# Kernel tuning notes

Measured on AMD Instinct MI355X. Metric: run time of the kernel, lower is better.

The kernel has to match this reference:

```python
import jax, jax.numpy as jnp
import numpy as np

TOP_K = 2


def setup_inputs() -> dict:
    key = jax.random.key(0)
    k0, k1, k2, k3 = jax.random.split(key, 4)
    B, S, H, I, E = 4, 2048, 1024, 2048, 8
    x = jax.random.normal(k0, (B, S, H), dtype=jnp.float32)
    Wr = jax.random.normal(k1, (H, E), dtype=jnp.float32) * 0.02
    W1 = jax.random.normal(k2, (E, H, 2 * I), dtype=jnp.float32) * 0.02
    W2 = jax.random.normal(k3, (E, I, H), dtype=jnp.float32) * 0.02
    return {"x": x, "Wr": Wr, "W1": W1, "W2": W2}


def reference(x, Wr, W1, W2):
    B, S, H = x.shape
    E = W1.shape[0]
    I = W2.shape[1]
    xf = x.reshape(-1, H)  # [T, H], T = B*S

    # Top-k router
    logits = xf @ Wr                              # [T, E]
    probs = jax.nn.softmax(logits, axis=-1)
    rw, sel = jax.lax.top_k(probs, TOP_K)          # [T, k], [T, k]
    rw = rw.astype(jnp.float32)
    rw = rw / rw.sum(axis=-1, keepdims=True)

    out = jnp.zeros_like(xf)
    for e in range(E):
        # combined gate weight for this expert per token (0 if not routed here)
        g = (rw * (sel == e)).sum(axis=-1)         # [T]
        h = xf @ W1[e]                             # [T, 2I]
        gate, up = h[:, :I], h[:, I:]
        eo = (jax.nn.silu(gate) * up) @ W2[e]      # [T, H]
        out = out + g[:, None] * eo
    return out.reshape(B, S, H)
```

## Files before the change

### kernel.cpp

```cpp
#include <hip/hip_runtime.h>
#include <hip/hip_bf16.h>

#define NTOK   8192
#define HDIM   1024
#define NEXP   8
#define IDIM   2048
#define TOTAL  (NTOK*2)

typedef short bf16x8 __attribute__((ext_vector_type(8)));
typedef float f32x4  __attribute__((ext_vector_type(4)));

__device__ __forceinline__ unsigned short f2bf(float f) {
  __hip_bfloat16 h = __float2bfloat16(f);
  return *reinterpret_cast<unsigned short*>(&h);
}
__device__ __forceinline__ float bf2f(unsigned short u) {
  __hip_bfloat16 h = *reinterpret_cast<__hip_bfloat16*>(&u);
  return __bfloat162float(h);
}

__device__ __forceinline__ void lds_load16(const unsigned short* gsrc, unsigned short* lds_base_uniform) {
  __builtin_amdgcn_global_load_lds(
      (const __attribute__((address_space(1))) unsigned int*)gsrc,
      (__attribute__((address_space(3))) unsigned int*)lds_base_uniform,
      16, 0, 0);
}

__global__ void router_kernel(const float* __restrict__ x, const float* __restrict__ Wr,
                              int* __restrict__ sel, float* __restrict__ selw,
                              int* __restrict__ counts) {
  int t = blockIdx.x * 4 + (threadIdx.x >> 6);
  int lane = threadIdx.x & 63;
  float acc[NEXP];
#pragma unroll
  for (int e = 0; e < NEXP; ++e) acc[e] = 0.f;
  const float* xr = x + (size_t)t * HDIM;
  for (int h = lane; h < HDIM; h += 64) {
    float xv = xr[h];
    const float* wr = Wr + h * NEXP;
#pragma unroll
    for (int e = 0; e < NEXP; ++e) acc[e] += xv * wr[e];
  }
#pragma unroll
  for (int off = 32; off > 0; off >>= 1) {
#pragma unroll
    for (int e = 0; e < NEXP; ++e) acc[e] += __shfl_xor(acc[e], off, 64);
  }
  if (lane == 0) {
    int i0 = 0; float v0 = acc[0];
#pragma unroll
    for (int e = 1; e < NEXP; ++e) if (acc[e] > v0) { v0 = acc[e]; i0 = e; }
    int i1 = -1; float v1 = -1e30f;
#pragma unroll
    for (int e = 0; e < NEXP; ++e) if (e != i0 && acc[e] > v1) { v1 = acc[e]; i1 = e; }
    float e1 = expf(v1 - v0);
    float w0 = 1.f / (1.f + e1);
    float w1 = e1 / (1.f + e1);
    sel[t*2] = i0; sel[t*2+1] = i1;
    selw[t*2] = w0; selw[t*2+1] = w1;
    atomicAdd(&counts[i0], 1);
    atomicAdd(&counts[i1], 1);
  }
}

__global__ void prefix_kernel(const int* __restrict__ counts, int* __restrict__ offsets,
                              int* __restrict__ cursor) {
  if (threadIdx.x == 0) {
    int s = 0;
    for (int e = 0; e < NEXP; ++e) { offsets[e] = s; cursor[e] = s; s += counts[e]; }
    offsets[NEXP] = s;
  }
}

__global__ void scatter_kernel(const int* __restrict__ sel, const float* __restrict__ selw,
                               int* __restrict__ cursor, int* __restrict__ token_ids,
                               float* __restrict__ gates) {
  int t = blockIdx.x * 256 + threadIdx.x;
  if (t >= NTOK) return;
#pragma unroll
  for (int k = 0; k < 2; ++k) {
    int e = sel[t*2+k];
    int p = atomicAdd(&cursor[e], 1);
    token_ids[p] = t;
    gates[p] = selw[t*2+k];
  }
}

__global__ void xsplit_kernel(const float* __restrict__ x, unsigned short* __restrict__ Xs) {
  int t = blockIdx.x;
  const float4* src = reinterpret_cast<const float4*>(x + (size_t)t * HDIM);
  float4 v = src[threadIdx.x];
  unsigned short h0 = f2bf(v.x), h1 = f2bf(v.y), h2 = f2bf(v.z), h3 = f2bf(v.w);
  ushort4 hi = { h0, h1, h2, h3 };
  ushort4 lo = { f2bf(v.x - bf2f(h0)), f2bf(v.y - bf2f(h1)),
                 f2bf(v.z - bf2f(h2)), f2bf(v.w - bf2f(h3)) };
  *reinterpret_cast<ushort4*>(Xs + (size_t)t*2*HDIM + threadIdx.x*4) = hi;
  *reinterpret_cast<ushort4*>(Xs + (size_t)t*2*HDIM + HDIM + threadIdx.x*4) = lo;
}

__global__ void split_transpose_kernel(const float* __restrict__ W, unsigned short* __restrict__ WT,
                                       int R, int C) {
  int e = blockIdx.z;
  int c0 = blockIdx.x * 64, r0 = blockIdx.y * 64;
  __shared__ unsigned short hiT[64][65];
  __shared__ unsigned short loT[64][65];
  int tx = threadIdx.x & 63, ty = threadIdx.x >> 6;
  const float* src = W + ((size_t)e * R + r0) * C + c0;
#pragma unroll
  for (int rr = 0; rr < 16; ++rr) {
    int r_l = ty * 16 + rr;
    float v = src[(size_t)r_l * C + tx];
    unsigned short h = f2bf(v);
    hiT[tx][r_l] = h;
    loT[tx][r_l] = f2bf(v - bf2f(h));
  }
  __syncthreads();
  unsigned short* dst = WT + ((size_t)e * C + c0) * (size_t)(2*R) + r0;
#pragma unroll
  for (int ww = 0; ww < 16; ++ww) {
    int c_l = ty * 16 + ww;
    dst[(size_t)c_l * (2*R) + tx]     = hiT[c_l][tx];
    dst[(size_t)c_l * (2*R) + R + tx] = loT[c_l][tx];
  }
}

__global__ __launch_bounds__(256, 2)
void gemm1_kernel(const unsigned short* __restrict__ Xs,
                  const unsigned short* __restrict__ W1sT,
                  unsigned short* __restrict__ actS,
                  const int* __restrict__ offsets,
                  const int* __restrict__ token_ids) {
  int e = blockIdx.z;
  int off = offsets[e];
  int cnt = offsets[e+1] - off;
  int r0 = blockIdx.x * 128;
  if (r0 >= cnt) return;
  int j0 = blockIdx.y * 128;

  __shared__ unsigned short As[128*64];
  __shared__ unsigned short Bg[128*64];
  __shared__ unsigned short Bu[128*64];

  int tid = threadIdx.x;
  int lane = tid & 63, wv = tid >> 6;
  int l15 = lane & 15, lq = lane >> 4;
  int lr = lane >> 3;
  int g  = lane & 7;
  int wr = wv >> 1;
  int wc = wv & 1;

  const unsigned short* w1e = W1sT + (size_t)e * 4096 * 2048;

  const unsigned short* srcA[4]; unsigned short* dstA[4];
  const unsigned short* srcBg[4]; const unsigned short* srcBu[4];
  unsigned short* dstBg[4]; unsigned short* dstBu[4];
#pragma unroll
  for (int i = 0; i < 4; ++i) {
    int rowt = wv*32 + i*8 + lr;
    int gp = off + r0 + rowt; if (gp > TOTAL-1) gp = TOTAL-1;
    int tok = token_ids[gp];
    int sg = g ^ (rowt & 7);
    srcA[i] = Xs + (size_t)tok*2048 + sg*8;
    dstA[i] = As + wv*2048 + i*512;
    srcBg[i] = w1e + (size_t)(j0 + rowt)*2048 + sg*8;
    srcBu[i] = w1e + (size_t)(IDIM + j0 + rowt)*2048 + sg*8;
    dstBg[i] = Bg + wv*2048 + i*512;
    dstBu[i] = Bu + wv*2048 + i*512;
  }

  f32x4 accg[4][4], accu[4][4];
#pragma unroll
  for (int m = 0; m < 4; ++m)
#pragma unroll
    for (int n = 0; n < 4; ++n) {
      accg[m][n] = f32x4{0.f, 0.f, 0.f, 0.f};
      accu[m][n] = f32x4{0.f, 0.f, 0.f, 0.f};
    }

  for (int ks = 0; ks < 48; ++ks) {
    int s  = ks >> 4;
    int k0 = (ks & 15) << 6;
    int aoff = ((s == 1) ? HDIM : 0) + k0;
    int boff = ((s == 2) ? HDIM : 0) + k0;

#pragma unroll
    for (int i = 0; i < 4; ++i) lds_load16(srcA[i] + aoff, dstA[i]);
#pragma unroll
    for (int i = 0; i < 4; ++i) {
      lds_load16(srcBg[i] + boff, dstBg[i]);
      lds_load16(srcBu[i] + boff, dstBu[i]);
    }
    __syncthreads();

#pragma unroll
    for (int kk = 0; kk < 2; ++kk) {
      int gg = ((kk*4 + lq) ^ (l15 & 7)) * 8;
      bf16x8 af[4], bgf[4], buf2[4];
#pragma unroll
      for (int m = 0; m < 4; ++m)
        af[m] = *reinterpret_cast<const bf16x8*>(&As[(wr*64 + m*16 + l15)*64 + gg]);
#pragma unroll
      for (int n = 0; n < 4; ++n) {
        bgf[n]  = *reinterpret_cast<const bf16x8*>(&Bg[(wc*64 + n*16 + l15)*64 + gg]);
        buf2[n] = *reinterpret_cast<const bf16x8*>(&Bu[(wc*64 + n*16 + l15)*64 + gg]);
      }
#pragma unroll
      for (int m = 0; m < 4; ++m)
#pragma unroll
        for (int n = 0; n < 4; ++n) {
          accg[m][n] = __builtin_amdgcn_mfma_f32_16x16x32_bf16(af[m], bgf[n], accg[m][n], 0, 0, 0);
          accu[m][n] = __builtin_amdgcn_mfma_f32_16x16x32_bf16(af[m], buf2[n], accu[m][n], 0, 0, 0);
        }
    }
    __syncthreads();
  }

#pragma unroll
  for (int m = 0; m < 4; ++m) {
#pragma unroll
    for (int rr = 0; rr < 4; ++rr) {
      int lrow = r0 + wr*64 + m*16 + lq*4 + rr;
      if (lrow < cnt) {
        size_t prow = (size_t)(off + lrow);
#pragma unroll
        for (int n = 0; n < 4; ++n) {
          float gte = accg[m][n][rr], u = accu[m][n][rr];
          float a = (gte / (1.f + expf(-gte))) * u;
          unsigned short hh = f2bf(a);
          unsigned short ll = f2bf(a - bf2f(hh));
          int col = j0 + wc*64 + n*16 + l15;
          actS[prow*4096 + col]        = hh;
          actS[prow*4096 + IDIM + col] = ll;
        }
      }
    }
  }
}

__global__ __launch_bounds__(256, 2)
void gemm2_kernel(const unsigned short* __restrict__ actS,
                  const unsigned short* __restrict__ W2sT,
                  const int* __restrict__ offsets,
                  const int* __restrict__ token_ids,
                  const float* __restrict__ gates,
                  float* __restrict__ out) {
  int e = blockIdx.z;
  int off = offsets[e];
  int cnt = offsets[e+1] - off;
  int r0 = blockIdx.x * 128;
  if (r0 >= cnt) return;
  int c0 = blockIdx.y * 256;

  __shared__ unsigned short As[128*64];
  __shared__ unsigned short Bs[256*64];

  int tid = threadIdx.x;
  int lane = tid & 63, wv = tid >> 6;
  int l15 = lane & 15, lq = lane >> 4;
  int lr = lane >> 3;
  int g  = lane & 7;
  int wr = wv >> 1;
  int wc = wv & 1;

  const unsigned short* w2e = W2sT + (size_t)e * 1024 * 4096;

  const unsigned short* srcA[4]; unsigned short* dstA[4];
  const unsigned short* srcB[8]; unsigned short* dstB[8];
#pragma unroll
  for (int i = 0; i < 4; ++i) {
    int rowt = wv*32 + i*8 + lr;
    int gp = off + r0 + rowt; if (gp > TOTAL-1) gp = TOTAL-1;
    int sg = g ^ (rowt & 7);
    srcA[i] = actS + (size_t)gp*4096 + sg*8;
    dstA[i] = As + wv*2048 + i*512;
  }
#pragma unroll
  for (int i = 0; i < 8; ++i) {
    int rowt = wv*64 + i*8 + lr;
    int sg = g ^ (rowt & 7);
    srcB[i] = w2e + (size_t)(c0 + rowt)*4096 + sg*8;
    dstB[i] = Bs + wv*4096 + i*512;
  }

  f32x4 acc[4][8];
#pragma unroll
  for (int m = 0; m < 4; ++m)
#pragma unroll
    for (int n = 0; n < 8; ++n) acc[m][n] = f32x4{0.f, 0.f, 0.f, 0.f};

  for (int ks = 0; ks < 96; ++ks) {
    int s  = ks >> 5;
    int k0 = (ks & 31) << 6;
    int aoff = ((s == 1) ? IDIM : 0) + k0;
    int boff = ((s == 2) ? IDIM : 0) + k0;

#pragma unroll
    for (int i = 0; i < 4; ++i) lds_load16(srcA[i] + aoff, dstA[i]);
#pragma unroll
    for (int i = 0; i < 8; ++i) lds_load16(srcB[i] + boff, dstB[i]);
    __syncthreads();

#pragma unroll
    for (int kk = 0; kk < 2; ++kk) {
      int gg = ((kk*4 + lq) ^ (l15 & 7)) * 8;
      bf16x8 af[4], bfr[8];
#pragma unroll
      for (int m = 0; m < 4; ++m)
        af[m] = *reinterpret_cast<const bf16x8*>(&As[(wr*64 + m*16 + l15)*64 + gg]);
#pragma unroll
      for (int n = 0; n < 8; ++n)
        bfr[n] = *reinterpret_cast<const bf16x8*>(&Bs[(wc*128 + n*16 + l15)*64 + gg]);
#pragma unroll
      for (int m = 0; m < 4; ++m)
#pragma unroll
        for (int n = 0; n < 8; ++n)
          acc[m][n] = __builtin_amdgcn_mfma_f32_16x16x32_bf16(af[m], bfr[n], acc[m][n], 0, 0, 0);
    }
    __syncthreads();
  }

#pragma unroll
  for (int m = 0; m < 4; ++m) {
#pragma unroll
    for (int rr = 0; rr < 4; ++rr) {
      int lrow = r0 + wr*64 + m*16 + lq*4 + rr;
      if (lrow < cnt) {
        int pos = off + lrow;
        int t = token_ids[pos];
        float w = gates[pos];
        float* orow = out + (size_t)t * HDIM;
#pragma unroll
        for (int n = 0; n < 8; ++n)
          atomicAdd(&orow[c0 + wc*128 + n*16 + l15], w * acc[m][n][rr]);
      }
    }
  }
}

extern "C" void kernel_launch(void* const* d_in, const int* in_sizes, int n_in,
                              void* d_out, int out_size, void* d_ws, size_t ws_size,
                              hipStream_t stream) {
  (void)in_sizes; (void)n_in;
  const float* x  = (const float*)d_in[0];
  const float* Wr = (const float*)d_in[1];
  const float* W1 = (const float*)d_in[2];
  const float* W2 = (const float*)d_in[3];
  float* out = (float*)d_out;

  char* ws = (char*)d_ws;
  int*   counts    = (int*)(ws + 0);
  int*   offsets   = (int*)(ws + 64);
  int*   cursor    = (int*)(ws + 128);
  int*   sel       = (int*)(ws + 4096);
  float* selw      = (float*)(ws + 4096 + 65536);
  int*   token_ids = (int*)(ws + 4096 + 2*65536);
  float* gates     = (float*)(ws + 4096 + 3*65536);
  const size_t XS_OFF   = 266240ULL;
  const size_t W1T_OFF  = XS_OFF  + 33554432ULL;
  const size_t W2T_OFF  = W1T_OFF + 134217728ULL;
  const size_t ACT_OFF  = W2T_OFF + 67108864ULL;
  const size_t REQUIRED = ACT_OFF + 134217728ULL;
  unsigned short* Xs   = (unsigned short*)(ws + XS_OFF);
  unsigned short* W1sT = (unsigned short*)(ws + W1T_OFF);
  unsigned short* W2sT = (unsigned short*)(ws + W2T_OFF);
  unsigned short* actS = (unsigned short*)(ws + ACT_OFF);

  hipMemsetAsync(d_out, 0, (size_t)out_size * sizeof(float), stream);
  if (ws_size < REQUIRED) return;

  hipMemsetAsync(counts, 0, 64, stream);
  router_kernel<<<NTOK/4, 256, 0, stream>>>(x, Wr, sel, selw, counts);
  prefix_kernel<<<1, 64, 0, stream>>>(counts, offsets, cursor);
  scatter_kernel<<<NTOK/256, 256, 0, stream>>>(sel, selw, cursor, token_ids, gates);
  xsplit_kernel<<<NTOK, 256, 0, stream>>>(x, Xs);
  split_transpose_kernel<<<dim3(64, 16, NEXP), 256, 0, stream>>>(W1, W1sT, 1024, 4096);
  split_transpose_kernel<<<dim3(16, 32, NEXP), 256, 0, stream>>>(W2, W2sT, 2048, 1024);
  gemm1_kernel<<<dim3(64, 16, NEXP), 256, 0, stream>>>(Xs, W1sT, actS, offsets, token_ids);
  gemm2_kernel<<<dim3(64, 4, NEXP), 256, 0, stream>>>(actS, W2sT, offsets, token_ids, gates, out);
}
```

Baseline: 1.660 ms.

## Double-buffer GEMM LDS stages and launch a compacted per-expert tile list

Both expert GEMMs now use two LDS buffers with a K-step of 32 and a single barrier per step. The next stage's global-to-LDS load is issued before the MFMAs on the current buffer, so load latency overlaps with compute. The prefix kernel also builds a compact list of (expert, row-tile) pairs, which replaces the old 64×8 grid in which most blocks exited immediately. The costs are twice as many loop iterations and barriers, a narrower XOR swizzle that may raise LDS bank conflicts, and a fixed MAXT bound on the tile count.

```diff
diff --git a/kernel.cpp b/kernel.cpp
--- a/kernel.cpp
+++ b/kernel.cpp
@@ -6,6 +6,7 @@
 #define NEXP   8
 #define IDIM   2048
 #define TOTAL  (NTOK*2)
+#define MAXT   136
 
 typedef short bf16x8 __attribute__((ext_vector_type(8)));
 typedef float f32x4  __attribute__((ext_vector_type(4)));
@@ -64,11 +65,16 @@
 }
 
 __global__ void prefix_kernel(const int* __restrict__ counts, int* __restrict__ offsets,
-                              int* __restrict__ cursor) {
+                              int* __restrict__ cursor, int* __restrict__ tile_e,
+                              int* __restrict__ tile_r) {
   if (threadIdx.x == 0) {
     int s = 0;
     for (int e = 0; e < NEXP; ++e) { offsets[e] = s; cursor[e] = s; s += counts[e]; }
     offsets[NEXP] = s;
+    int nt = 0;
+    for (int e = 0; e < NEXP; ++e)
+      for (int r0 = 0; r0 < counts[e]; r0 += 128) { tile_e[nt] = e; tile_r[nt] = r0; ++nt; }
+    for (; nt < MAXT; ++nt) { tile_e[nt] = -1; tile_r[nt] = 0; }
   }
 }
 
@@ -129,44 +135,59 @@
                   const unsigned short* __restrict__ W1sT,
                   unsigned short* __restrict__ actS,
                   const int* __restrict__ offsets,
-                  const int* __restrict__ token_ids) {
-  int e = blockIdx.z;
+                  const int* __restrict__ token_ids,
+                  const int* __restrict__ tile_e,
+                  const int* __restrict__ tile_r) {
+  int e = tile_e[blockIdx.x];
+  if (e < 0) return;
+  int r0 = tile_r[blockIdx.x];
   int off = offsets[e];
   int cnt = offsets[e+1] - off;
-  int r0 = blockIdx.x * 128;
-  if (r0 >= cnt) return;
   int j0 = blockIdx.y * 128;
 
-  __shared__ unsigned short As[128*64];
-  __shared__ unsigned short Bg[128*64];
-  __shared__ unsigned short Bu[128*64];
+  __shared__ unsigned short As[2*128*32];
+  __shared__ unsigned short Bg[2*128*32];
+  __shared__ unsigned short Bu[2*128*32];
 
   int tid = threadIdx.x;
   int lane = tid & 63, wv = tid >> 6;
   int l15 = lane & 15, lq = lane >> 4;
-  int lr = lane >> 3;
-  int g  = lane & 7;
+  int lr = lane >> 2;
+  int g2 = lane & 3;
   int wr = wv >> 1;
   int wc = wv & 1;
 
   const unsigned short* w1e = W1sT + (size_t)e * 4096 * 2048;
 
-  const unsigned short* srcA[4]; unsigned short* dstA[4];
-  const unsigned short* srcBg[4]; const unsigned short* srcBu[4];
-  unsigned short* dstBg[4]; unsigned short* dstBu[4];
-#pragma unroll
-  for (int i = 0; i < 4; ++i) {
-    int rowt = wv*32 + i*8 + lr;
+  const unsigned short* srcA[2]; unsigned short* dstA[2];
+  const unsigned short* srcBg[2]; const unsigned short* srcBu[2];
+  unsigned short* dstBg[2]; unsigned short* dstBu[2];
+#pragma unroll
+  for (int i = 0; i < 2; ++i) {
+    int rowt = wv*32 + i*16 + lr;
     int gp = off + r0 + rowt; if (gp > TOTAL-1) gp = TOTAL-1;
     int tok = token_ids[gp];
-    int sg = g ^ (rowt & 7);
-    srcA[i] = Xs + (size_t)tok*2048 + sg*8;
-    dstA[i] = As + wv*2048 + i*512;
+    int sg = g2 ^ (rowt & 3);
+    srcA[i]  = Xs + (size_t)tok*2048 + sg*8;
+    dstA[i]  = As + wv*1024 + i*512;
     srcBg[i] = w1e + (size_t)(j0 + rowt)*2048 + sg*8;
     srcBu[i] = w1e + (size_t)(IDIM + j0 + rowt)*2048 + sg*8;
-    dstBg[i] = Bg + wv*2048 + i*512;
-    dstBu[i] = Bu + wv*2048 + i*512;
-  }
+    dstBg[i] = Bg + wv*1024 + i*512;
+    dstBu[i] = Bu + wv*1024 + i*512;
+  }
+
+#define G1_STAGE(ks, par) do {                                          \
+    int s_ = (ks) >> 5; int k0_ = ((ks) & 31) << 5;                     \
+    int aoff_ = ((s_ == 1) ? HDIM : 0) + k0_;                           \
+    int boff_ = ((s_ == 2) ? HDIM : 0) + k0_;                           \
+    int po_ = (par) * 4096;                                             \
+    _Pragma("unroll")                                                   \
+    for (int i_ = 0; i_ < 2; ++i_) {                                    \
+      lds_load16(srcA[i_]  + aoff_, dstA[i_]  + po_);                   \
+      lds_load16(srcBg[i_] + boff_, dstBg[i_] + po_);                   \
+      lds_load16(srcBu[i_] + boff_, dstBu[i_] + po_);                   \
+    }                                                                   \
+  } while (0)
 
   f32x4 accg[4][4], accu[4][4];
 #pragma unroll
@@ -177,43 +198,34 @@
       accu[m][n] = f32x4{0.f, 0.f, 0.f, 0.f};
     }
 
-  for (int ks = 0; ks < 48; ++ks) {
-    int s  = ks >> 4;
-    int k0 = (ks & 15) << 6;
-    int aoff = ((s == 1) ? HDIM : 0) + k0;
-    int boff = ((s == 2) ? HDIM : 0) + k0;
-
-#pragma unroll
-    for (int i = 0; i < 4; ++i) lds_load16(srcA[i] + aoff, dstA[i]);
-#pragma unroll
-    for (int i = 0; i < 4; ++i) {
-      lds_load16(srcBg[i] + boff, dstBg[i]);
-      lds_load16(srcBu[i] + boff, dstBu[i]);
+  int gg = (lq ^ (l15 & 3)) * 8;
+
+  G1_STAGE(0, 0);
+  int cur = 0;
+  for (int ks = 0; ks < 96; ++ks) {
+    __syncthreads();
+    if (ks + 1 < 96) G1_STAGE(ks + 1, cur ^ 1);
+
+    int po = cur * 4096;
+    bf16x8 af[4], bgf[4], buf2[4];
+#pragma unroll
+    for (int m = 0; m < 4; ++m)
+      af[m] = *reinterpret_cast<const bf16x8*>(&As[po + (wr*64 + m*16 + l15)*32 + gg]);
+#pragma unroll
+    for (int n = 0; n < 4; ++n) {
+      bgf[n]  = *reinterpret_cast<const bf16x8*>(&Bg[po + (wc*64 + n*16 + l15)*32 + gg]);
+      buf2[n] = *reinterpret_cast<const bf16x8*>(&Bu[po + (wc*64 + n*16 + l15)*32 + gg]);
     }
-    __syncthreads();
-
-#pragma unroll
-    for (int kk = 0; kk < 2; ++kk) {
-      int gg = ((kk*4 + lq) ^ (l15 & 7)) * 8;
-      bf16x8 af[4], bgf[4], buf2[4];
-#pragma unroll
-      for (int m = 0; m < 4; ++m)
-        af[m] = *reinterpret_cast<const bf16x8*>(&As[(wr*64 + m*16 + l15)*64 + gg]);
+#pragma unroll
+    for (int m = 0; m < 4; ++m)
 #pragma unroll
       for (int n = 0; n < 4; ++n) {
-        bgf[n]  = *reinterpret_cast<const bf16x8*>(&Bg[(wc*64 + n*16 + l15)*64 + gg]);
-        buf2[n] = *reinterpret_cast<const bf16x8*>(&Bu[(wc*64 + n*16 + l15)*64 + gg]);
+        accg[m][n] = __builtin_amdgcn_mfma_f32_16x16x32_bf16(af[m], bgf[n], accg[m][n], 0, 0, 0);
+        accu[m][n] = __builtin_amdgcn_mfma_f32_16x16x32_bf16(af[m], buf2[n], accu[m][n], 0, 0, 0);
       }
-#pragma unroll
-      for (int m = 0; m < 4; ++m)
-#pragma unroll
-        for (int n = 0; n < 4; ++n) {
-          accg[m][n] = __builtin_amdgcn_mfma_f32_16x16x32_bf16(af[m], bgf[n], accg[m][n], 0, 0, 0);
-          accu[m][n] = __builtin_amdgcn_mfma_f32_16x16x32_bf16(af[m], buf2[n], accu[m][n], 0, 0, 0);
-        }
-    }
-    __syncthreads();
-  }
+    cur ^= 1;
+  }
+#undef G1_STAGE
 
 #pragma unroll
   for (int m = 0; m < 4; ++m) {
@@ -243,44 +255,57 @@
                   const int* __restrict__ offsets,
                   const int* __restrict__ token_ids,
                   const float* __restrict__ gates,
-                  float* __restrict__ out) {
-  int e = blockIdx.z;
+                  float* __restrict__ out,
+                  const int* __restrict__ tile_e,
+                  const int* __restrict__ tile_r) {
+  int e = tile_e[blockIdx.x];
+  if (e < 0) return;
+  int r0 = tile_r[blockIdx.x];
   int off = offsets[e];
   int cnt = offsets[e+1] - off;
-  int r0 = blockIdx.x * 128;
-  if (r0 >= cnt) return;
   int c0 = blockIdx.y * 256;
 
-  __shared__ unsigned short As[128*64];
-  __shared__ unsigned short Bs[256*64];
+  __shared__ unsigned short As[2*128*32];
+  __shared__ unsigned short Bs[2*256*32];
 
   int tid = threadIdx.x;
   int lane = tid & 63, wv = tid >> 6;
   int l15 = lane & 15, lq = lane >> 4;
-  int lr = lane >> 3;
-  int g  = lane & 7;
+  int lr = lane >> 2;
+  int g2 = lane & 3;
   int wr = wv >> 1;
   int wc = wv & 1;
 
   const unsigned short* w2e = W2sT + (size_t)e * 1024 * 4096;
 
-  const unsigned short* srcA[4]; unsigned short* dstA[4];
-  const unsigned short* srcB[8]; unsigned short* dstB[8];
+  const unsigned short* srcA[2]; unsigned short* dstA[2];
+  const unsigned short* srcB[4]; unsigned short* dstB[4];
+#pragma unroll
+  for (int i = 0; i < 2; ++i) {
+    int rowt = wv*32 + i*16 + lr;
+    int gp = off + r0 + rowt; if (gp > TOTAL-1) gp = TOTAL-1;
+    int sg = g2 ^ (rowt & 3);
+    srcA[i] = actS + (size_t)gp*4096 + sg*8;
+    dstA[i] = As + wv*1024 + i*512;
+  }
 #pragma unroll
   for (int i = 0; i < 4; ++i) {
-    int rowt = wv*32 + i*8 + lr;
-    int gp = off + r0 + rowt; if (gp > TOTAL-1) gp = TOTAL-1;
-    int sg = g ^ (rowt & 7);
-    srcA[i] = actS + (size_t)gp*4096 + sg*8;
-    dstA[i] = As + wv*2048 + i*512;
-  }
-#pragma unroll
-  for (int i = 0; i < 8; ++i) {
-    int rowt = wv*64 + i*8 + lr;
-    int sg = g ^ (rowt & 7);
+    int rowt = wv*64 + i*16 + lr;
+    int sg = g2 ^ (rowt & 3);
     srcB[i] = w2e + (size_t)(c0 + rowt)*4096 + sg*8;
-    dstB[i] = Bs + wv*4096 + i*512;
-  }
+    dstB[i] = Bs + wv*2048 + i*512;
+  }
+
+#define G2_STAGE(ks, par) do {                                          \
+    int s_ = (ks) >> 6; int k0_ = ((ks) & 63) << 5;                     \
+    int aoff_ = ((s_ == 1) ? IDIM : 0) + k0_;                           \
+    int boff_ = ((s_ == 2) ? IDIM : 0) + k0_;                           \
+    int poA_ = (par) * 4096; int poB_ = (par) * 8192;                   \
+    _Pragma("unroll")                                                   \
+    for (int i_ = 0; i_ < 2; ++i_) lds_load16(srcA[i_] + aoff_, dstA[i_] + poA_); \
+    _Pragma("unroll")                                                   \
+    for (int i_ = 0; i_ < 4; ++i_) lds_load16(srcB[i_] + boff_, dstB[i_] + poB_); \
+  } while (0)
 
   f32x4 acc[4][8];
 #pragma unroll
@@ -288,36 +313,30 @@
 #pragma unroll
     for (int n = 0; n < 8; ++n) acc[m][n] = f32x4{0.f, 0.f, 0.f, 0.f};
 
-  for (int ks = 0; ks < 96; ++ks) {
-    int s  = ks >> 5;
-    int k0 = (ks & 31) << 6;
-    int aoff = ((s == 1) ? IDIM : 0) + k0;
-    int boff = ((s == 2) ? IDIM : 0) + k0;
-
-#pragma unroll
-    for (int i = 0; i < 4; ++i) lds_load16(srcA[i] + aoff, dstA[i]);
-#pragma unroll
-    for (int i = 0; i < 8; ++i) lds_load16(srcB[i] + boff, dstB[i]);
+  int gg = (lq ^ (l15 & 3)) * 8;
+
+  G2_STAGE(0, 0);
+  int cur = 0;
+  for (int ks = 0; ks < 192; ++ks) {
     __syncthreads();
-
-#pragma unroll
-    for (int kk = 0; kk < 2; ++kk) {
-      int gg = ((kk*4 + lq) ^ (l15 & 7)) * 8;
-      bf16x8 af[4], bfr[8];
-#pragma unroll
-      for (int m = 0; m < 4; ++m)
-        af[m] = *reinterpret_cast<const bf16x8*>(&As[(wr*64 + m*16 + l15)*64 + gg]);
+    if (ks + 1 < 192) G2_STAGE(ks + 1, cur ^ 1);
+
+    int poA = cur * 4096, poB = cur * 8192;
+    bf16x8 af[4], bfr[8];
+#pragma unroll
+    for (int m = 0; m < 4; ++m)
+      af[m] = *reinterpret_cast<const bf16x8*>(&As[poA + (wr*64 + m*16 + l15)*32 + gg]);
+#pragma unroll
+    for (int n = 0; n < 8; ++n)
+      bfr[n] = *reinterpret_cast<const bf16x8*>(&Bs[poB + (wc*128 + n*16 + l15)*32 + gg]);
+#pragma unroll
+    for (int m = 0; m < 4; ++m)
 #pragma unroll
       for (int n = 0; n < 8; ++n)
-        bfr[n] = *reinterpret_cast<const bf16x8*>(&Bs[(wc*128 + n*16 + l15)*64 + gg]);
-#pragma unroll
-      for (int m = 0; m < 4; ++m)
-#pragma unroll
-        for (int n = 0; n < 8; ++n)
-          acc[m][n] = __builtin_amdgcn_mfma_f32_16x16x32_bf16(af[m], bfr[n], acc[m][n], 0, 0, 0);
-    }
-    __syncthreads();
-  }
+        acc[m][n] = __builtin_amdgcn_mfma_f32_16x16x32_bf16(af[m], bfr[n], acc[m][n], 0, 0, 0);
+    cur ^= 1;
+  }
+#undef G2_STAGE
 
 #pragma unroll
   for (int m = 0; m < 4; ++m) {
@@ -351,6 +370,8 @@
   int*   counts    = (int*)(ws + 0);
   int*   offsets   = (int*)(ws + 64);
   int*   cursor    = (int*)(ws + 128);
+  int*   tile_e    = (int*)(ws + 192);
+  int*   tile_r    = (int*)(ws + 768);
   int*   sel       = (int*)(ws + 4096);
   float* selw      = (float*)(ws + 4096 + 65536);
   int*   token_ids = (int*)(ws + 4096 + 2*65536);
@@ -370,11 +391,11 @@
 
   hipMemsetAsync(counts, 0, 64, stream);
   router_kernel<<<NTOK/4, 256, 0, stream>>>(x, Wr, sel, selw, counts);
-  prefix_kernel<<<1, 64, 0, stream>>>(counts, offsets, cursor);
+  prefix_kernel<<<1, 64, 0, stream>>>(counts, offsets, cursor, tile_e, tile_r);
   scatter_kernel<<<NTOK/256, 256, 0, stream>>>(sel, selw, cursor, token_ids, gates);
   xsplit_kernel<<<NTOK, 256, 0, stream>>>(x, Xs);
   split_transpose_kernel<<<dim3(64, 16, NEXP), 256, 0, stream>>>(W1, W1sT, 1024, 4096);
   split_transpose_kernel<<<dim3(16, 32, NEXP), 256, 0, stream>>>(W2, W2sT, 2048, 1024);
-  gemm1_kernel<<<dim3(64, 16, NEXP), 256, 0, stream>>>(Xs, W1sT, actS, offsets, token_ids);
-  gemm2_kernel<<<dim3(64, 4, NEXP), 256, 0, stream>>>(actS, W2sT, offsets, token_ids, gates, out);
-}
+  gemm1_kernel<<<dim3(MAXT, 16, 1), 256, 0, stream>>>(Xs, W1sT, actS, offsets, token_ids, tile_e, tile_r);
+  gemm2_kernel<<<dim3(MAXT, 4, 1), 256, 0, stream>>>(actS, W2sT, offsets, token_ids, gates, out, tile_e, tile_r);
+}
```

After: 1.734 ms. +4.5%, slower.
